# Performance work log

Hardware: AMD Instinct MI355X
Metric: run time of the kernel (lower is better)

## Reference

```python
import jax, jax.numpy as jnp
import numpy as np

HEADS = 8
DIM_HEAD = 64
INNER = HEADS * DIM_HEAD  # 512
QUERY_DIM = 512
CONTEXT_DIM = 512


def setup_inputs() -> dict:
    key = jax.random.key(0)
    ks = jax.random.split(key, 10)
    s_in = 1.0 / np.sqrt(QUERY_DIM)
    s_ctx = 1.0 / np.sqrt(CONTEXT_DIM)
    s_o = 1.0 / np.sqrt(INNER)
    return {
        "x": jax.random.normal(ks[0], (8, QUERY_DIM, 32, 32), jnp.float32),
        "context": jax.random.normal(ks[1], (8, CONTEXT_DIM, 32, 32), jnp.float32),
        "Wq": jax.random.normal(ks[2], (INNER, QUERY_DIM), jnp.float32) * s_in,
        "bq": jnp.zeros((INNER,), jnp.float32),
        "Wk": jax.random.normal(ks[3], (INNER, CONTEXT_DIM), jnp.float32) * s_ctx,
        "bk": jnp.zeros((INNER,), jnp.float32),
        "Wv": jax.random.normal(ks[4], (INNER, CONTEXT_DIM), jnp.float32) * s_ctx,
        "bv": jnp.zeros((INNER,), jnp.float32),
        "Wo": jax.random.normal(ks[5], (QUERY_DIM, INNER), jnp.float32) * s_o,
        "bo": jnp.zeros((QUERY_DIM,), jnp.float32),
    }


def _proj1x1(t, W, b):
    # 1x1 Conv2d: channel mixing only. t: [B,Cin,X,Y], W: [Cout,Cin]
    return jnp.einsum('bcxy,oc->boxy', t, W) + b[None, :, None, None]


def reference(x, context, Wq, bq, Wk, bk, Wv, bv, Wo, bo):
    b, c, h, w = x.shape
    scale = DIM_HEAD ** (-0.5)

    q = _proj1x1(x, Wq, bq)
    k = _proj1x1(context, Wk, bk)
    v = _proj1x1(context, Wv, bv)

    def split_heads(t):
        B, C, X, Y = t.shape  # C = HEADS*DIM_HEAD
        return t.reshape(B, HEADS, DIM_HEAD, X * Y)  # b h d n

    q = split_heads(q) * scale
    k = split_heads(k)
    v = split_heads(v)

    sim = jnp.einsum('bhdi,bhdj->bhij', q, k)          # [b,h,i,j]
    attn = jax.nn.softmax(sim, axis=-1)
    out = jnp.einsum('bhij,bhdj->bhid', attn, v)       # [b,h,i,d]
    # rearrange 'b h (x y) d -> b (h d) x y'
    out = out.transpose(0, 1, 3, 2).reshape(b, HEADS * DIM_HEAD, h, w)
    return _proj1x1(out, Wo, bo)
```

## Files before the change

### kernel.cpp

```cpp
#include <hip/hip_runtime.h>
#include <stdint.h>

#define NB   8
#define CH   512
#define NPIX 1024
#define DH   64

typedef float  f32x4  __attribute__((ext_vector_type(4)));
typedef float  f32x16 __attribute__((ext_vector_type(16)));
typedef __bf16 bf16x8 __attribute__((ext_vector_type(8)));
typedef unsigned int u32x4 __attribute__((ext_vector_type(4)));

static __device__ __forceinline__ unsigned short f2bf(float f) {
    unsigned int u = __builtin_bit_cast(unsigned int, f);
    u += 0x7FFFu + ((u >> 16) & 1u);
    return (unsigned short)(u >> 16);
}

static __device__ __forceinline__ bf16x8 ld_bf8(const unsigned short* p) {
    return *reinterpret_cast<const bf16x8*>(p);
}

static __device__ __forceinline__ unsigned int cvtpk_bf16(float lo, float hi) {
    unsigned int r;
    asm("v_cvt_pk_bf16_f32 %0,%1,%2" : "=v"(r) : "v"(lo), "v"(hi));
    return r;
}

static __device__ __forceinline__ float fexp2(float x) {
    float r;
    asm("v_exp_f32 %0, %1" : "=v"(r) : "v"(x));
    return r;
}

static __device__ __forceinline__ void plswap(unsigned int& a, unsigned int& b) {
    asm("v_permlane32_swap_b32 %0, %1" : "+v"(a), "+v"(b));
}

static __device__ __forceinline__ void glds16(const unsigned short* g, void* l) {
    __builtin_amdgcn_global_load_lds(
        (const __attribute__((address_space(1))) unsigned int*)g,
        (__attribute__((address_space(3))) unsigned int*)l,
        16, 0, 0);
}

#define WAIT_VMCNT_8() asm volatile("s_waitcnt vmcnt(8)" ::: "memory")
#define WAIT_VMCNT_4() asm volatile("s_waitcnt vmcnt(4)" ::: "memory")
#define WAIT_VMCNT_0() asm volatile("s_waitcnt vmcnt(0)" ::: "memory")
#define WAIT_LGKM_0()  asm volatile("s_waitcnt lgkmcnt(0)" ::: "memory")

__global__ __launch_bounds__(256) void wconv_kernel(
        const float* __restrict__ Wq, const float* __restrict__ Wk,
        const float* __restrict__ Wv, const float* __restrict__ Wo,
        unsigned short* __restrict__ out) {
    int idx = blockIdx.x * 256 + threadIdx.x;
    int which = idx >> 18;
    int off   = idx & 0x3FFFF;
    const float* src = which == 0 ? Wq : which == 1 ? Wk : which == 2 ? Wv : Wo;
    out[idx] = f2bf(src[off]);
}

__global__ __launch_bounds__(256) void tconv_kernel(
        const float* __restrict__ x, const float* __restrict__ ctx,
        unsigned short* __restrict__ XT, unsigned short* __restrict__ CT) {
    __shared__ float tile[32][33];
    const int z = blockIdx.z;
    const float* src = (z < 8) ? x : ctx;
    unsigned short* dst = (z < 8) ? XT : CT;
    const int b  = z & 7;
    const int c0 = blockIdx.x * 32, n0 = blockIdx.y * 32;
    const int t  = threadIdx.x;
    const int r  = t >> 3, ch4 = (t & 7) * 4;
    const float* s = src + (size_t)b * CH * NPIX + (size_t)(c0 + r) * NPIX + n0 + ch4;
    float4 v4 = *(const float4*)s;
    tile[r][ch4] = v4.x; tile[r][ch4 + 1] = v4.y;
    tile[r][ch4 + 2] = v4.z; tile[r][ch4 + 3] = v4.w;
    __syncthreads();
    unsigned int lo = ((unsigned)f2bf(tile[ch4 + 1][r]) << 16) | f2bf(tile[ch4][r]);
    unsigned int hw = ((unsigned)f2bf(tile[ch4 + 3][r]) << 16) | f2bf(tile[ch4 + 2][r]);
    *(uint2*)(dst + (size_t)b * NPIX * CH + (size_t)(n0 + r) * CH + c0 + ch4)
        = make_uint2(lo, hw);
}

static __device__ __forceinline__ void gemm128(
        const unsigned short* __restrict__ Wp,
        const unsigned short* __restrict__ Xp,
        f32x4 acc[4][4]) {
    __shared__ __align__(16) unsigned short lA[2][128][32];
    __shared__ __align__(16) unsigned short lB[2][128][32];
    const int tid  = threadIdx.x;
    const int lane = tid & 63;
    const int wv   = tid >> 6;
    const int wm   = wv & 1, wn = tid >> 7;

    const unsigned short* gA = Wp + (size_t)(wv * 32 + (lane >> 2)) * CH + (lane & 3) * 8;
    const unsigned short* gB = Xp + (size_t)(wv * 32 + (lane >> 2)) * CH + (lane & 3) * 8;

    auto stage = [&](int kt, int buf) {
        const int k0 = kt * 32;
        char* dA = (char*)&lA[buf][0][0] + wv * 2048;
        char* dB = (char*)&lB[buf][0][0] + wv * 2048;
        glds16(gA + k0,           dA);
        glds16(gA + k0 + 16 * CH, dA + 1024);
        glds16(gB + k0,           dB);
        glds16(gB + k0 + 16 * CH, dB + 1024);
    };

    stage(0, 0);
    stage(1, 1);

#pragma unroll 1
    for (int kt = 0; kt < 16; kt++) {
        if (kt < 15) { WAIT_VMCNT_4(); } else { WAIT_VMCNT_0(); }
        __builtin_amdgcn_s_barrier();
        const int buf = kt & 1;
        bf16x8 af[4], bfrag[4];
#pragma unroll
        for (int i = 0; i < 4; i++)
            af[i] = ld_bf8(&lA[buf][wm * 64 + i * 16 + (lane & 15)][(lane >> 4) * 8]);
#pragma unroll
        for (int j = 0; j < 4; j++)
            bfrag[j] = ld_bf8(&lB[buf][wn * 64 + j * 16 + (lane & 15)][(lane >> 4) * 8]);
#pragma unroll
        for (int i = 0; i < 4; i++)
#pragma unroll
            for (int j = 0; j < 4; j++)
                acc[i][j] = __builtin_amdgcn_mfma_f32_16x16x32_bf16(af[i], bfrag[j], acc[i][j], 0, 0, 0);
        WAIT_LGKM_0();
        __builtin_amdgcn_s_barrier();
        if (kt + 2 < 16) stage(kt + 2, buf);
    }
}

__global__ __launch_bounds__(256) void proj_qkv_kernel(
        const unsigned short* __restrict__ XT, const unsigned short* __restrict__ CT,
        const unsigned short* __restrict__ Wbf,
        const float* __restrict__ bq, const float* __restrict__ bk, const float* __restrict__ bv,
        unsigned short* __restrict__ Q, unsigned short* __restrict__ K, unsigned short* __restrict__ V) {
    const int z = blockIdx.z;
    const int b = z / 3, mode = z - 3 * b;
    const int o0 = blockIdx.x * 128, n0 = blockIdx.y * 128;
    const unsigned short* W = Wbf + (size_t)mode * CH * CH;
    const unsigned short* X = (mode == 0 ? XT : CT) + (size_t)b * NPIX * CH;
    const float* bias = mode == 0 ? bq : mode == 1 ? bk : bv;

    f32x4 acc[4][4];
#pragma unroll
    for (int i = 0; i < 4; i++)
#pragma unroll
        for (int j = 0; j < 4; j++)
#pragma unroll
            for (int r = 0; r < 4; r++) acc[i][j][r] = 0.f;

    gemm128(W + (size_t)o0 * CH, X + (size_t)n0 * CH, acc);

    const int lane = threadIdx.x & 63;
    const int wm = (threadIdx.x >> 6) & 1, wn = threadIdx.x >> 7;
    const float qs = 0.125f * 1.44269504088896340736f;
#pragma unroll
    for (int i = 0; i < 4; i++) {
        const int ob = o0 + wm * 64 + i * 16 + (lane >> 4) * 4;
        const int h = ob >> 6, dd = ob & 63;
        float b4[4];
#pragma unroll
        for (int r = 0; r < 4; r++) b4[r] = bias[ob + r];
#pragma unroll
        for (int j = 0; j < 4; j++) {
            const int n = n0 + wn * 64 + j * 16 + (lane & 15);
            float v[4];
#pragma unroll
            for (int r = 0; r < 4; r++) v[r] = acc[i][j][r] + b4[r];
            if (mode == 0) {
#pragma unroll
                for (int r = 0; r < 4; r++) v[r] *= qs;
            }
            if (mode <= 1) {
                unsigned int lo = (unsigned)f2bf(v[0]) | ((unsigned)f2bf(v[1]) << 16);
                unsigned int hi = (unsigned)f2bf(v[2]) | ((unsigned)f2bf(v[3]) << 16);
                unsigned short* dst = (mode == 0 ? Q : K) +
                    (((size_t)(b * 8 + h) * NPIX) + n) * DH + dd;
                *(uint2*)dst = make_uint2(lo, hi);
            } else {
#pragma unroll
                for (int r = 0; r < 4; r++)
                    V[(((size_t)(b * 8 + h) * 32 + (n >> 5)) * 64 + dd + r) * 32 + (n & 31)]
                        = f2bf(v[r]);
            }
        }
    }
}

__global__ __launch_bounds__(64) void attn_kernel(
        const unsigned short* __restrict__ Qg, const unsigned short* __restrict__ Kg,
        const unsigned short* __restrict__ Vg, unsigned short* __restrict__ AT) {
    __shared__ __align__(16) unsigned short ldsK[2][2048];
    __shared__ __align__(16) unsigned short ldsV[2][2048];

    const int p  = blockIdx.x;
    const int local = p >> 3;
    const int bh = ((p & 7) << 3) | (local >> 5);
    const int qb = local & 31;
    const int q0 = qb * 32;
    const int lane = threadIdx.x;
    const int lq = lane & 31, hi = lane >> 5;

    const unsigned short* Qb = Qg + ((size_t)bh * NPIX + q0 + lq) * DH + hi * 8;
    bf16x8 qf[4];
#pragma unroll
    for (int ds = 0; ds < 4; ds++) qf[ds] = ld_bf8(Qb + ds * 16);

    f32x16 o0, o1, zro;
#pragma unroll
    for (int r = 0; r < 16; r++) { o0[r] = 0.f; o1[r] = 0.f; zro[r] = 0.f; }
    float l_run = 0.f;

    const int swzK = (((lane & 7) ^ ((lane >> 3) & 7)) << 3);
    const unsigned short* gK = Kg + ((size_t)bh * NPIX + (lane >> 3)) * DH + swzK;
    const int swzV = (((lane & 3) ^ ((lane >> 2) & 3)) << 3);
    const unsigned short* gV = Vg + (size_t)bh * 32 * 2048 + (size_t)(lane >> 2) * 32 + swzV;

    auto stage = [&](int t, int buf) {
        const unsigned short* sk = gK + (size_t)t * 32 * DH;
        char* dK = (char*)&ldsK[buf][0];
        glds16(sk,           dK);
        glds16(sk +  8 * DH, dK + 1024);
        glds16(sk + 16 * DH, dK + 2048);
        glds16(sk + 24 * DH, dK + 3072);
        const unsigned short* sv = gV + (size_t)t * 2048;
        char* dV = (char*)&ldsV[buf][0];
        glds16(sv,        dV);
        glds16(sv +  512, dV + 1024);
        glds16(sv + 1024, dV + 2048);
        glds16(sv + 1536, dV + 3072);
    };

    stage(0, 0);
    stage(1, 1);

    const int lql7 = lq & 7, lql3 = lq & 3;
#pragma unroll 1
    for (int t = 0; t < 32; ++t) {
        if (t < 31) { WAIT_VMCNT_8(); } else { WAIT_VMCNT_0(); }
        const int cur = t & 1;
        const unsigned short* kb = &ldsK[cur][0] + lq * 64;
        bf16x8 kf0 = ld_bf8(kb + (((0 + hi) ^ lql7) << 3));
        bf16x8 kf1 = ld_bf8(kb + (((2 + hi) ^ lql7) << 3));
        bf16x8 kf2 = ld_bf8(kb + (((4 + hi) ^ lql7) << 3));
        bf16x8 kf3 = ld_bf8(kb + (((6 + hi) ^ lql7) << 3));

        f32x16 s;
        __builtin_amdgcn_s_setprio(1);
        s = __builtin_amdgcn_mfma_f32_32x32x16_bf16(kf0, qf[0], zro, 0, 0, 0);
        s = __builtin_amdgcn_mfma_f32_32x32x16_bf16(kf1, qf[1], s, 0, 0, 0);
        s = __builtin_amdgcn_mfma_f32_32x32x16_bf16(kf2, qf[2], s, 0, 0, 0);
        s = __builtin_amdgcn_mfma_f32_32x32x16_bf16(kf3, qf[3], s, 0, 0, 0);
        __builtin_amdgcn_s_setprio(0);

        const unsigned short* vb0 = &ldsV[cur][0] + lq * 32;
        const unsigned short* vb1 = vb0 + 32 * 32;
        bf16x8 v00 = ld_bf8(vb0 + (((0 + hi) ^ lql3) << 3));
        bf16x8 v01 = ld_bf8(vb0 + (((2 + hi) ^ lql3) << 3));
        bf16x8 v10 = ld_bf8(vb1 + (((0 + hi) ^ lql3) << 3));
        bf16x8 v11 = ld_bf8(vb1 + (((2 + hi) ^ lql3) << 3));

#pragma unroll
        for (int r = 0; r < 16; r++) s[r] = fexp2(s[r]);
        float s8[8], s4[4];
#pragma unroll
        for (int i = 0; i < 8; i++) s8[i] = s[2 * i] + s[2 * i + 1];
#pragma unroll
        for (int i = 0; i < 4; i++) s4[i] = s8[2 * i] + s8[2 * i + 1];
        l_run += (s4[0] + s4[1]) + (s4[2] + s4[3]);

        bf16x8 pa[2];
#pragma unroll
        for (int ks = 0; ks < 2; ks++) {
            const int bse = ks * 8;
            unsigned int X0 = cvtpk_bf16(s[bse + 0], s[bse + 1]);
            unsigned int X1 = cvtpk_bf16(s[bse + 2], s[bse + 3]);
            unsigned int X2 = cvtpk_bf16(s[bse + 4], s[bse + 5]);
            unsigned int X3 = cvtpk_bf16(s[bse + 6], s[bse + 7]);
            plswap(X0, X2); plswap(X1, X3);
            u32x4 wv; wv[0] = X0; wv[1] = X1; wv[2] = X2; wv[3] = X3;
            pa[ks] = __builtin_bit_cast(bf16x8, wv);
        }

        __builtin_amdgcn_s_setprio(1);
        o0 = __builtin_amdgcn_mfma_f32_32x32x16_bf16(pa[0], v00, o0, 0, 0, 0);
        o1 = __builtin_amdgcn_mfma_f32_32x32x16_bf16(pa[0], v10, o1, 0, 0, 0);
        o0 = __builtin_amdgcn_mfma_f32_32x32x16_bf16(pa[1], v01, o0, 0, 0, 0);
        o1 = __builtin_amdgcn_mfma_f32_32x32x16_bf16(pa[1], v11, o1, 0, 0, 0);
        __builtin_amdgcn_s_setprio(0);

        __builtin_amdgcn_sched_barrier(0);
        if (t + 2 < 32) stage(t + 2, cur);
    }

    l_run += __shfl_xor(l_run, 32);
    float inv = 1.0f / l_run;
    const int b = bh >> 3, h = bh & 7;
#pragma unroll
    for (int r = 0; r < 16; r++) {
        int crow = (r & 3) + 8 * (r >> 2) + 4 * hi;
        float fac = __shfl(inv, crow);
        int q = q0 + crow;
        unsigned short* dst = AT + ((size_t)b * NPIX + q) * CH + h * 64 + lq;
        dst[0]  = f2bf(o0[r] * fac);
        dst[32] = f2bf(o1[r] * fac);
    }
}

__global__ __launch_bounds__(256) void proj_out_kernel(
        const unsigned short* __restrict__ AT, const unsigned short* __restrict__ Wo,
        const float* __restrict__ bo, float* __restrict__ out) {
    const int b = blockIdx.z;
    const int o0 = blockIdx.x * 128, n0 = blockIdx.y * 128;
    f32x4 acc[4][4];
#pragma unroll
    for (int i = 0; i < 4; i++)
#pragma unroll
        for (int j = 0; j < 4; j++)
#pragma unroll
            for (int r = 0; r < 4; r++) acc[i][j][r] = 0.f;

    gemm128(Wo + (size_t)o0 * CH, AT + ((size_t)b * NPIX + n0) * CH, acc);

    const int lane = threadIdx.x & 63;
    const int wm = (threadIdx.x >> 6) & 1, wn = threadIdx.x >> 7;
#pragma unroll
    for (int i = 0; i < 4; i++) {
        const int ob = o0 + wm * 64 + i * 16 + (lane >> 4) * 4;
        float b4[4];
#pragma unroll
        for (int r = 0; r < 4; r++) b4[r] = bo[ob + r];
#pragma unroll
        for (int j = 0; j < 4; j++) {
            const int n = n0 + wn * 64 + j * 16 + (lane & 15);
#pragma unroll
            for (int r = 0; r < 4; r++)
                out[((size_t)b * CH + ob + r) * NPIX + n] = acc[i][j][r] + b4[r];
        }
    }
}

extern "C" void kernel_launch(void* const* d_in, const int* in_sizes, int n_in,
                              void* d_out, int out_size, void* d_ws, size_t ws_size,
                              hipStream_t stream) {
    const float* x   = (const float*)d_in[0];
    const float* ctx = (const float*)d_in[1];
    const float* Wq  = (const float*)d_in[2];
    const float* bq  = (const float*)d_in[3];
    const float* Wk  = (const float*)d_in[4];
    const float* bk  = (const float*)d_in[5];
    const float* Wv  = (const float*)d_in[6];
    const float* bv  = (const float*)d_in[7];
    const float* Wo  = (const float*)d_in[8];
    const float* bo  = (const float*)d_in[9];
    float* out = (float*)d_out;

    char* ws = (char*)d_ws;
    unsigned short* XT  = (unsigned short*)(ws);
    unsigned short* CT  = (unsigned short*)(ws + 8388608);
    unsigned short* Wbf = (unsigned short*)(ws + 16777216);
    unsigned short* Q   = (unsigned short*)(ws + 18874368);
    unsigned short* K   = (unsigned short*)(ws + 27262976);
    unsigned short* V   = (unsigned short*)(ws + 35651584);
    unsigned short* AT  = XT;

    wconv_kernel<<<4096, 256, 0, stream>>>(Wq, Wk, Wv, Wo, Wbf);
    tconv_kernel<<<dim3(16, 32, 16), 256, 0, stream>>>(x, ctx, XT, CT);
    proj_qkv_kernel<<<dim3(4, 8, 24), 256, 0, stream>>>(XT, CT, Wbf, bq, bk, bv, Q, K, V);
    attn_kernel<<<2048, 64, 0, stream>>>(Q, K, V, AT);
    proj_out_kernel<<<dim3(4, 8, 8), 256, 0, stream>>>(AT, Wbf + 3 * 262144, bo, out);
}
```

Before: 94.23 us.

## Process 64 queries per attention block with two waves splitting keys

The attention kernel now gives each block 64 queries and two waves; each wave takes half of the keys and reuses every loaded K/V tile for two 32-query groups. The partial outputs and row sums are combined through LDS at the end. The V layout written by the projection kernel is changed to a 64-wide swizzled row format that matches the new LDS reads. Projection grids are flattened to 1D with the batch index in the low bits, which changes block ordering for L2 locality. This halves K/V traffic per query but adds register pressure and an LDS reduction step.

```diff
diff --git a/kernel.cpp b/kernel.cpp
--- a/kernel.cpp
+++ b/kernel.cpp
@@ -137,9 +137,9 @@
         const unsigned short* __restrict__ Wbf,
         const float* __restrict__ bq, const float* __restrict__ bk, const float* __restrict__ bv,
         unsigned short* __restrict__ Q, unsigned short* __restrict__ K, unsigned short* __restrict__ V) {
-    const int z = blockIdx.z;
-    const int b = z / 3, mode = z - 3 * b;
-    const int o0 = blockIdx.x * 128, n0 = blockIdx.y * 128;
+    const int id = blockIdx.x;
+    const int b = id & 7, mode = id >> 8, inner = (id >> 3) & 31;
+    const int o0 = (inner & 3) * 128, n0 = (inner >> 2) * 128;
     const unsigned short* W = Wbf + (size_t)mode * CH * CH;
     const unsigned short* X = (mode == 0 ? XT : CT) + (size_t)b * NPIX * CH;
     const float* bias = mode == 0 ? bq : mode == 1 ? bk : bv;
@@ -182,52 +182,60 @@
                 *(uint2*)dst = make_uint2(lo, hi);
             } else {
 #pragma unroll
-                for (int r = 0; r < 4; r++)
-                    V[(((size_t)(b * 8 + h) * 32 + (n >> 5)) * 64 + dd + r) * 32 + (n & 31)]
-                        = f2bf(v[r]);
+                for (int r = 0; r < 4; r++) {
+                    int d = dd + r;
+                    V[(((size_t)(b * 8 + h) * 32 + (n >> 5)) * 2048)
+                      + (size_t)(d & 31) * 64 + (d >> 5) * 32 + (n & 31)] = f2bf(v[r]);
+                }
             }
         }
     }
 }
 
-__global__ __launch_bounds__(64) void attn_kernel(
+__global__ __launch_bounds__(128) void attn_kernel(
         const unsigned short* __restrict__ Qg, const unsigned short* __restrict__ Kg,
         const unsigned short* __restrict__ Vg, unsigned short* __restrict__ AT) {
-    __shared__ __align__(16) unsigned short ldsK[2][2048];
-    __shared__ __align__(16) unsigned short ldsV[2][2048];
+    __shared__ __align__(16) unsigned short ldsS[2][2][2][2048];
+    __shared__ float lbuf[64];
 
     const int p  = blockIdx.x;
     const int local = p >> 3;
-    const int bh = ((p & 7) << 3) | (local >> 5);
-    const int qb = local & 31;
-    const int q0 = qb * 32;
-    const int lane = threadIdx.x;
-    const int lq = lane & 31, hi = lane >> 5;
-
-    const unsigned short* Qb = Qg + ((size_t)bh * NPIX + q0 + lq) * DH + hi * 8;
-    bf16x8 qf[4];
-#pragma unroll
-    for (int ds = 0; ds < 4; ds++) qf[ds] = ld_bf8(Qb + ds * 16);
-
-    f32x16 o0, o1, zro;
-#pragma unroll
-    for (int r = 0; r < 16; r++) { o0[r] = 0.f; o1[r] = 0.f; zro[r] = 0.f; }
-    float l_run = 0.f;
-
-    const int swzK = (((lane & 7) ^ ((lane >> 3) & 7)) << 3);
-    const unsigned short* gK = Kg + ((size_t)bh * NPIX + (lane >> 3)) * DH + swzK;
-    const int swzV = (((lane & 3) ^ ((lane >> 2) & 3)) << 3);
-    const unsigned short* gV = Vg + (size_t)bh * 32 * 2048 + (size_t)(lane >> 2) * 32 + swzV;
+    const int bh = ((p & 7) << 3) | (local >> 4);
+    const int qb = local & 15;
+    const int q0 = qb * 64;
+    const int tid = threadIdx.x, wave = tid >> 6, lane = tid & 63;
+    const int lq = lane & 31, hi = lane >> 5, lql7 = lq & 7;
+    const int key0 = wave * 512;
+
+    const unsigned short* Qp = Qg + ((size_t)bh * NPIX + q0 + lq) * DH + hi * 8;
+    bf16x8 qa[4], qbf[4];
+#pragma unroll
+    for (int ds = 0; ds < 4; ds++) {
+        qa[ds]  = ld_bf8(Qp + ds * 16);
+        qbf[ds] = ld_bf8(Qp + 32 * DH + ds * 16);
+    }
+
+    f32x16 oA0, oA1, oB0, oB1, zro;
+#pragma unroll
+    for (int r = 0; r < 16; r++) {
+        oA0[r] = 0.f; oA1[r] = 0.f; oB0[r] = 0.f; oB1[r] = 0.f; zro[r] = 0.f;
+    }
+    float lA = 0.f, lB = 0.f;
+
+    const int swz = (((lane & 7) ^ ((lane >> 3) & 7)) << 3);
+    const unsigned short* gK = Kg + ((size_t)bh * NPIX + key0 + (lane >> 3)) * DH + swz;
+    const unsigned short* gV = Vg + (size_t)bh * 65536 + (size_t)(key0 >> 5) * 2048
+                                  + (lane >> 3) * 64 + swz;
 
     auto stage = [&](int t, int buf) {
         const unsigned short* sk = gK + (size_t)t * 32 * DH;
-        char* dK = (char*)&ldsK[buf][0];
+        char* dK = (char*)&ldsS[wave][buf][0][0];
         glds16(sk,           dK);
         glds16(sk +  8 * DH, dK + 1024);
         glds16(sk + 16 * DH, dK + 2048);
         glds16(sk + 24 * DH, dK + 3072);
         const unsigned short* sv = gV + (size_t)t * 2048;
-        char* dV = (char*)&ldsV[buf][0];
+        char* dV = (char*)&ldsS[wave][buf][1][0];
         glds16(sv,        dV);
         glds16(sv +  512, dV + 1024);
         glds16(sv + 1024, dV + 2048);
@@ -237,84 +245,124 @@
     stage(0, 0);
     stage(1, 1);
 
-    const int lql7 = lq & 7, lql3 = lq & 3;
 #pragma unroll 1
-    for (int t = 0; t < 32; ++t) {
-        if (t < 31) { WAIT_VMCNT_8(); } else { WAIT_VMCNT_0(); }
+    for (int t = 0; t < 16; ++t) {
+        if (t < 15) { WAIT_VMCNT_8(); } else { WAIT_VMCNT_0(); }
         const int cur = t & 1;
-        const unsigned short* kb = &ldsK[cur][0] + lq * 64;
+        const unsigned short* kb = &ldsS[wave][cur][0][0] + lq * 64;
         bf16x8 kf0 = ld_bf8(kb + (((0 + hi) ^ lql7) << 3));
         bf16x8 kf1 = ld_bf8(kb + (((2 + hi) ^ lql7) << 3));
         bf16x8 kf2 = ld_bf8(kb + (((4 + hi) ^ lql7) << 3));
         bf16x8 kf3 = ld_bf8(kb + (((6 + hi) ^ lql7) << 3));
 
-        f32x16 s;
+        f32x16 sA, sB;
         __builtin_amdgcn_s_setprio(1);
-        s = __builtin_amdgcn_mfma_f32_32x32x16_bf16(kf0, qf[0], zro, 0, 0, 0);
-        s = __builtin_amdgcn_mfma_f32_32x32x16_bf16(kf1, qf[1], s, 0, 0, 0);
-        s = __builtin_amdgcn_mfma_f32_32x32x16_bf16(kf2, qf[2], s, 0, 0, 0);
-        s = __builtin_amdgcn_mfma_f32_32x32x16_bf16(kf3, qf[3], s, 0, 0, 0);
+        sA = __builtin_amdgcn_mfma_f32_32x32x16_bf16(kf0, qa[0],  zro, 0, 0, 0);
+        sB = __builtin_amdgcn_mfma_f32_32x32x16_bf16(kf0, qbf[0], zro, 0, 0, 0);
+        sA = __builtin_amdgcn_mfma_f32_32x32x16_bf16(kf1, qa[1],  sA, 0, 0, 0);
+        sB = __builtin_amdgcn_mfma_f32_32x32x16_bf16(kf1, qbf[1], sB, 0, 0, 0);
+        sA = __builtin_amdgcn_mfma_f32_32x32x16_bf16(kf2, qa[2],  sA, 0, 0, 0);
+        sB = __builtin_amdgcn_mfma_f32_32x32x16_bf16(kf2, qbf[2], sB, 0, 0, 0);
+        sA = __builtin_amdgcn_mfma_f32_32x32x16_bf16(kf3, qa[3],  sA, 0, 0, 0);
+        sB = __builtin_amdgcn_mfma_f32_32x32x16_bf16(kf3, qbf[3], sB, 0, 0, 0);
         __builtin_amdgcn_s_setprio(0);
 
-        const unsigned short* vb0 = &ldsV[cur][0] + lq * 32;
-        const unsigned short* vb1 = vb0 + 32 * 32;
-        bf16x8 v00 = ld_bf8(vb0 + (((0 + hi) ^ lql3) << 3));
-        bf16x8 v01 = ld_bf8(vb0 + (((2 + hi) ^ lql3) << 3));
-        bf16x8 v10 = ld_bf8(vb1 + (((0 + hi) ^ lql3) << 3));
-        bf16x8 v11 = ld_bf8(vb1 + (((2 + hi) ^ lql3) << 3));
-
-#pragma unroll
-        for (int r = 0; r < 16; r++) s[r] = fexp2(s[r]);
-        float s8[8], s4[4];
-#pragma unroll
-        for (int i = 0; i < 8; i++) s8[i] = s[2 * i] + s[2 * i + 1];
-#pragma unroll
-        for (int i = 0; i < 4; i++) s4[i] = s8[2 * i] + s8[2 * i + 1];
-        l_run += (s4[0] + s4[1]) + (s4[2] + s4[3]);
-
-        bf16x8 pa[2];
+        const unsigned short* vb = &ldsS[wave][cur][1][0] + lq * 64;
+        bf16x8 v00 = ld_bf8(vb + (((0 + hi) ^ lql7) << 3));
+        bf16x8 v01 = ld_bf8(vb + (((2 + hi) ^ lql7) << 3));
+        bf16x8 v10 = ld_bf8(vb + (((4 + hi) ^ lql7) << 3));
+        bf16x8 v11 = ld_bf8(vb + (((6 + hi) ^ lql7) << 3));
+
+#pragma unroll
+        for (int r = 0; r < 16; r++) { sA[r] = fexp2(sA[r]); sB[r] = fexp2(sB[r]); }
+        {
+            float a8[8], b8[8], a4[4], b4[4];
+#pragma unroll
+            for (int i = 0; i < 8; i++) { a8[i] = sA[2*i] + sA[2*i+1]; b8[i] = sB[2*i] + sB[2*i+1]; }
+#pragma unroll
+            for (int i = 0; i < 4; i++) { a4[i] = a8[2*i] + a8[2*i+1]; b4[i] = b8[2*i] + b8[2*i+1]; }
+            lA += (a4[0] + a4[1]) + (a4[2] + a4[3]);
+            lB += (b4[0] + b4[1]) + (b4[2] + b4[3]);
+        }
+
+        bf16x8 paA[2], paB[2];
 #pragma unroll
         for (int ks = 0; ks < 2; ks++) {
             const int bse = ks * 8;
-            unsigned int X0 = cvtpk_bf16(s[bse + 0], s[bse + 1]);
-            unsigned int X1 = cvtpk_bf16(s[bse + 2], s[bse + 3]);
-            unsigned int X2 = cvtpk_bf16(s[bse + 4], s[bse + 5]);
-            unsigned int X3 = cvtpk_bf16(s[bse + 6], s[bse + 7]);
+            unsigned int X0 = cvtpk_bf16(sA[bse + 0], sA[bse + 1]);
+            unsigned int X1 = cvtpk_bf16(sA[bse + 2], sA[bse + 3]);
+            unsigned int X2 = cvtpk_bf16(sA[bse + 4], sA[bse + 5]);
+            unsigned int X3 = cvtpk_bf16(sA[bse + 6], sA[bse + 7]);
             plswap(X0, X2); plswap(X1, X3);
-            u32x4 wv; wv[0] = X0; wv[1] = X1; wv[2] = X2; wv[3] = X3;
-            pa[ks] = __builtin_bit_cast(bf16x8, wv);
+            u32x4 wa; wa[0] = X0; wa[1] = X1; wa[2] = X2; wa[3] = X3;
+            paA[ks] = __builtin_bit_cast(bf16x8, wa);
+            unsigned int Y0 = cvtpk_bf16(sB[bse + 0], sB[bse + 1]);
+            unsigned int Y1 = cvtpk_bf16(sB[bse + 2], sB[bse + 3]);
+            unsigned int Y2 = cvtpk_bf16(sB[bse + 4], sB[bse + 5]);
+            unsigned int Y3 = cvtpk_bf16(sB[bse + 6], sB[bse + 7]);
+            plswap(Y0, Y2); plswap(Y1, Y3);
+            u32x4 wb; wb[0] = Y0; wb[1] = Y1; wb[2] = Y2; wb[3] = Y3;
+            paB[ks] = __builtin_bit_cast(bf16x8, wb);
         }
 
         __builtin_amdgcn_s_setprio(1);
-        o0 = __builtin_amdgcn_mfma_f32_32x32x16_bf16(pa[0], v00, o0, 0, 0, 0);
-        o1 = __builtin_amdgcn_mfma_f32_32x32x16_bf16(pa[0], v10, o1, 0, 0, 0);
-        o0 = __builtin_amdgcn_mfma_f32_32x32x16_bf16(pa[1], v01, o0, 0, 0, 0);
-        o1 = __builtin_amdgcn_mfma_f32_32x32x16_bf16(pa[1], v11, o1, 0, 0, 0);
+        oA0 = __builtin_amdgcn_mfma_f32_32x32x16_bf16(paA[0], v00, oA0, 0, 0, 0);
+        oB0 = __builtin_amdgcn_mfma_f32_32x32x16_bf16(paB[0], v00, oB0, 0, 0, 0);
+        oA1 = __builtin_amdgcn_mfma_f32_32x32x16_bf16(paA[0], v10, oA1, 0, 0, 0);
+        oB1 = __builtin_amdgcn_mfma_f32_32x32x16_bf16(paB[0], v10, oB1, 0, 0, 0);
+        oA0 = __builtin_amdgcn_mfma_f32_32x32x16_bf16(paA[1], v01, oA0, 0, 0, 0);
+        oB0 = __builtin_amdgcn_mfma_f32_32x32x16_bf16(paB[1], v01, oB0, 0, 0, 0);
+        oA1 = __builtin_amdgcn_mfma_f32_32x32x16_bf16(paA[1], v11, oA1, 0, 0, 0);
+        oB1 = __builtin_amdgcn_mfma_f32_32x32x16_bf16(paB[1], v11, oB1, 0, 0, 0);
         __builtin_amdgcn_s_setprio(0);
 
         __builtin_amdgcn_sched_barrier(0);
-        if (t + 2 < 32) stage(t + 2, cur);
-    }
-
-    l_run += __shfl_xor(l_run, 32);
-    float inv = 1.0f / l_run;
-    const int b = bh >> 3, h = bh & 7;
-#pragma unroll
-    for (int r = 0; r < 16; r++) {
-        int crow = (r & 3) + 8 * (r >> 2) + 4 * hi;
-        float fac = __shfl(inv, crow);
-        int q = q0 + crow;
-        unsigned short* dst = AT + ((size_t)b * NPIX + q) * CH + h * 64 + lq;
-        dst[0]  = f2bf(o0[r] * fac);
-        dst[32] = f2bf(o1[r] * fac);
+        if (t + 2 < 16) stage(t + 2, cur);
+    }
+
+    lA += __shfl_xor(lA, 32);
+    lB += __shfl_xor(lB, 32);
+    float* obuf = (float*)&ldsS[1][0][0][0];
+    if (wave == 1) {
+#pragma unroll
+        for (int r = 0; r < 16; r++) {
+            obuf[(0 * 16 + r) * 64 + lane] = oA0[r];
+            obuf[(1 * 16 + r) * 64 + lane] = oA1[r];
+            obuf[(2 * 16 + r) * 64 + lane] = oB0[r];
+            obuf[(3 * 16 + r) * 64 + lane] = oB1[r];
+        }
+        if (lane < 32) { lbuf[lq] = lA; lbuf[32 + lq] = lB; }
+    }
+    __syncthreads();
+    if (wave == 0) {
+        float invA = 1.0f / (lA + lbuf[lq]);
+        float invB = 1.0f / (lB + lbuf[32 + lq]);
+        const int b = bh >> 3, h = bh & 7;
+#pragma unroll
+        for (int r = 0; r < 16; r++) {
+            float a0 = oA0[r] + obuf[(0 * 16 + r) * 64 + lane];
+            float a1 = oA1[r] + obuf[(1 * 16 + r) * 64 + lane];
+            float b0 = oB0[r] + obuf[(2 * 16 + r) * 64 + lane];
+            float b1 = oB1[r] + obuf[(3 * 16 + r) * 64 + lane];
+            int crow = (r & 3) + 8 * (r >> 2) + 4 * hi;
+            float facA = __shfl(invA, crow);
+            float facB = __shfl(invB, crow);
+            unsigned short* dA = AT + ((size_t)b * NPIX + q0 + crow) * CH + h * 64 + lq;
+            dA[0]  = f2bf(a0 * facA);
+            dA[32] = f2bf(a1 * facA);
+            unsigned short* dB = AT + ((size_t)b * NPIX + q0 + 32 + crow) * CH + h * 64 + lq;
+            dB[0]  = f2bf(b0 * facB);
+            dB[32] = f2bf(b1 * facB);
+        }
     }
 }
 
 __global__ __launch_bounds__(256) void proj_out_kernel(
         const unsigned short* __restrict__ AT, const unsigned short* __restrict__ Wo,
         const float* __restrict__ bo, float* __restrict__ out) {
-    const int b = blockIdx.z;
-    const int o0 = blockIdx.x * 128, n0 = blockIdx.y * 128;
+    const int id = blockIdx.x;
+    const int b = id & 7, inner = id >> 3;
+    const int o0 = (inner & 3) * 128, n0 = (inner >> 2) * 128;
     f32x4 acc[4][4];
 #pragma unroll
     for (int i = 0; i < 4; i++)
@@ -369,7 +417,7 @@
 
     wconv_kernel<<<4096, 256, 0, stream>>>(Wq, Wk, Wv, Wo, Wbf);
     tconv_kernel<<<dim3(16, 32, 16), 256, 0, stream>>>(x, ctx, XT, CT);
-    proj_qkv_kernel<<<dim3(4, 8, 24), 256, 0, stream>>>(XT, CT, Wbf, bq, bk, bv, Q, K, V);
-    attn_kernel<<<2048, 64, 0, stream>>>(Q, K, V, AT);
-    proj_out_kernel<<<dim3(4, 8, 8), 256, 0, stream>>>(AT, Wbf + 3 * 262144, bo, out);
-}
+    proj_qkv_kernel<<<768, 256, 0, stream>>>(XT, CT, Wbf, bq, bk, bv, Q, K, V);
+    attn_kernel<<<1024, 128, 0, stream>>>(Q, K, V, AT);
+    proj_out_kernel<<<256, 256, 0, stream>>>(AT, Wbf + 3 * 262144, bo, out);
+}
```

Result: faster. 84.79 us (-10.0%).
